# Performance work log

Measured on AMD Instinct MI355X. Metric: run time of the kernel, lower is better.

## Reference

```python
import jax, jax.numpy as jnp
import numpy as np

VOCAB = 50257
SOFT_CAP = 30.0
Z_LOSS_COEF = 1e-4
IGNORE_INDEX = -100


def setup_inputs() -> dict:
    key = jax.random.key(0)
    k1, k2, k3 = jax.random.split(key, 3)
    B, S, H = 2, 2048, 1024
    hidden = jax.random.normal(k1, (B, S, H), dtype=jnp.float32)
    lm_head_weight = jax.random.normal(k2, (VOCAB, H), dtype=jnp.float32) * 0.02
    labels = jax.random.randint(k3, (B, S), 0, VOCAB, dtype=jnp.int64)
    return {"hidden": hidden, "lm_head_weight": lm_head_weight, "labels": labels}


def reference(hidden, lm_head_weight, labels):
    # lm_head matmul: [B,S,H] x [V,H] -> [B,S,V]
    logits = jnp.einsum("bsh,vh->bsv", hidden, lm_head_weight)
    # Gemma-style tanh soft-cap
    logits = jnp.tanh(logits / SOFT_CAP) * SOFT_CAP
    # shift for next-token prediction
    shift_logits = logits[:, :-1].astype(jnp.float32)          # [B,S-1,V]
    shift_labels = labels[:, 1:]                               # [B,S-1]
    flat_logits = shift_logits.reshape(-1, VOCAB)              # [N,V]
    flat_labels = shift_labels.reshape(-1)                     # [N]
    valid = flat_labels != IGNORE_INDEX
    safe_labels = jnp.where(valid, flat_labels, 0)
    log_z = jax.nn.logsumexp(flat_logits, axis=-1)             # [N]
    picked = jnp.take_along_axis(flat_logits, safe_labels[:, None], axis=-1)[:, 0]
    nll = log_z - picked                                       # [N]
    n_valid = jnp.maximum(jnp.sum(valid), 1)
    ce = jnp.sum(jnp.where(valid, nll, 0.0)) / n_valid
    # z-loss: mean over valid tokens of logsumexp^2
    z_loss = ZLC = Z_LOSS_COEF * jnp.sum(jnp.where(valid, log_z ** 2, 0.0)) / n_valid
    return ce + z_loss
```

## Files before the change

kernel.cpp:

```cpp
#include <hip/hip_runtime.h>
#include <hip/hip_bf16.h>

#define VOCAB 50257
#define NPAD  50432
#define MROWS 4096
#define SEQ   2048
#define KDIM  1024
#define NT    16

typedef __attribute__((ext_vector_type(4))) float f32x4;
typedef __attribute__((ext_vector_type(8))) short bf16x8;

#define AS1 __attribute__((address_space(1)))
#define AS3 __attribute__((address_space(3)))

__device__ __forceinline__ void bar() {
  asm volatile("" ::: "memory");
  __builtin_amdgcn_s_barrier();
  asm volatile("" ::: "memory");
}

__device__ __forceinline__ unsigned int f2bf_pair(float lo, float hi) {
  unsigned int a = __float_as_uint(lo);
  a = (a + 0x7FFFu + ((a >> 16) & 1u)) >> 16;
  unsigned int b = __float_as_uint(hi);
  b = (b + 0x7FFFu + ((b >> 16) & 1u)) >> 16;
  return a | (b << 16);
}

__global__ void cast_hidden_k(const float* __restrict__ src, uint4* __restrict__ dst) {
  int i = blockIdx.x * 256 + threadIdx.x;
  const float4* s = ((const float4*)src) + (size_t)i * 2;
  float4 a = s[0], b = s[1];
  uint4 o;
  o.x = f2bf_pair(a.x, a.y);
  o.y = f2bf_pair(a.z, a.w);
  o.z = f2bf_pair(b.x, b.y);
  o.w = f2bf_pair(b.z, b.w);
  dst[i] = o;
}

__global__ void cast_weight_k(const float* __restrict__ src, uint4* __restrict__ dst) {
  int i = blockIdx.x * 256 + threadIdx.x;
  int row = i >> 7;
  uint4 o = make_uint4(0u, 0u, 0u, 0u);
  if (row < VOCAB) {
    const float4* s = ((const float4*)src) + (size_t)i * 2;
    float4 a = s[0], b = s[1];
    o.x = f2bf_pair(a.x, a.y);
    o.y = f2bf_pair(a.z, a.w);
    o.z = f2bf_pair(b.x, b.y);
    o.w = f2bf_pair(b.z, b.w);
  }
  dst[i] = o;
}

#define STAGE_X(base, h, bufb, isB, kt) do { \
  const unsigned short* _g = (base) + (size_t)((h)*128 + w*8) * KDIM + (kt)*64; \
  unsigned short* _l = LDS_ + (bufb) + (isB)*16384 + (h)*8192 + w*512; \
  __builtin_amdgcn_global_load_lds((const AS1 void*)_g, (AS3 void*)_l, 16, 0, 0); \
  __builtin_amdgcn_global_load_lds((const AS1 void*)(_g + (size_t)64*KDIM), (AS3 void*)(_l + 4096), 16, 0, 0); \
} while (0)

__global__ __launch_bounds__(512, 2) void gemm_ce_k(
    const unsigned short* __restrict__ A,
    const unsigned short* __restrict__ W,
    const int* __restrict__ labels,
    float* __restrict__ row_sum,
    float* __restrict__ picked)
{
  __shared__ __align__(16) unsigned short LDS_[65536];

  const int bid  = blockIdx.x;
  const int wg   = (bid & 7) * 394 + (bid >> 3);
  const int mblk = wg & 15;
  const int nblk = wg >> 4;
  const int tid  = threadIdx.x;
  const int lane = tid & 63;
  const int w    = tid >> 6;
  const int wm   = w >> 2;
  const int wn   = w & 3;

  const int arow0 = mblk * 256;
  const int wrow0 = nblk * 256;

  const int lrow = lane >> 3;
  const int lcol = ((lane & 7) * 8) ^ ((lane >> 3) << 3);
  const unsigned short* Abase = A + (size_t)(arow0 + lrow) * KDIM + lcol;
  const unsigned short* Wbase = W + (size_t)(wrow0 + lrow) * KDIM + lcol;

  const int rbase = (lane & 15) * 64 + (lane >> 4) * 8;
  const int xorm  = (lane & 7) << 3;

  f32x4 acc[8][4];
#pragma unroll
  for (int m = 0; m < 8; ++m)
#pragma unroll
    for (int n = 0; n < 4; ++n) acc[m][n] = (f32x4){0.f, 0.f, 0.f, 0.f};

  STAGE_X(Abase, 0, 0, 0, 0);
  STAGE_X(Abase, 1, 0, 0, 0);
  STAGE_X(Wbase, 0, 0, 1, 0);
  STAGE_X(Wbase, 1, 0, 1, 0);
  STAGE_X(Abase, 0, 32768, 0, 1);
  STAGE_X(Abase, 1, 32768, 0, 1);
  asm volatile("s_waitcnt vmcnt(4)" ::: "memory");
  bar();

  bf16x8 Af[2][4][2], Bf[2][2][2];

  for (int t = 0; t < NT; ++t) {
    const int cb = (t & 1) << 15;
    const int nb = cb ^ 32768;

#pragma unroll
    for (int a = 0; a < 4; ++a)
#pragma unroll
      for (int ks = 0; ks < 2; ++ks)
        Af[0][a][ks] = *(const bf16x8*)&LDS_[cb + (((wm*128 + a*16)*64 + rbase + ks*32) ^ xorm)];
#pragma unroll
    for (int b2 = 0; b2 < 2; ++b2)
#pragma unroll
      for (int ks = 0; ks < 2; ++ks)
        Bf[0][b2][ks] = *(const bf16x8*)&LDS_[cb + 16384 + (((wn*64 + b2*16)*64 + rbase + ks*32) ^ xorm)];
    if (t + 1 < NT) STAGE_X(Wbase, 0, nb, 1, t + 1);
    bar();
    __builtin_amdgcn_s_setprio(1);
#pragma unroll
    for (int a = 0; a < 4; ++a)
#pragma unroll
      for (int b2 = 0; b2 < 2; ++b2) {
        acc[a][b2] = __builtin_amdgcn_mfma_f32_16x16x32_bf16(Af[0][a][0], Bf[0][b2][0], acc[a][b2], 0, 0, 0);
        acc[a][b2] = __builtin_amdgcn_mfma_f32_16x16x32_bf16(Af[0][a][1], Bf[0][b2][1], acc[a][b2], 0, 0, 0);
      }
    __builtin_amdgcn_s_setprio(0);
    bar();

#pragma unroll
    for (int a = 0; a < 4; ++a)
#pragma unroll
      for (int ks = 0; ks < 2; ++ks)
        Af[1][a][ks] = *(const bf16x8*)&LDS_[cb + (((wm*128 + 64 + a*16)*64 + rbase + ks*32) ^ xorm)];
#pragma unroll
    for (int b2 = 0; b2 < 2; ++b2)
#pragma unroll
      for (int ks = 0; ks < 2; ++ks)
        Bf[1][b2][ks] = *(const bf16x8*)&LDS_[cb + 16384 + (((wn*64 + 32 + b2*16)*64 + rbase + ks*32) ^ xorm)];
    if (t + 1 < NT) STAGE_X(Wbase, 1, nb, 1, t + 1);
    bar();
    __builtin_amdgcn_s_setprio(1);
#pragma unroll
    for (int a = 0; a < 4; ++a)
#pragma unroll
      for (int b2 = 0; b2 < 2; ++b2) {
        acc[a][2+b2] = __builtin_amdgcn_mfma_f32_16x16x32_bf16(Af[0][a][0], Bf[1][b2][0], acc[a][2+b2], 0, 0, 0);
        acc[a][2+b2] = __builtin_amdgcn_mfma_f32_16x16x32_bf16(Af[0][a][1], Bf[1][b2][1], acc[a][2+b2], 0, 0, 0);
      }
    __builtin_amdgcn_s_setprio(0);
    bar();

    if (t + 2 < NT) STAGE_X(Abase, 0, cb, 0, t + 2);
    bar();
    __builtin_amdgcn_s_setprio(1);
#pragma unroll
    for (int a = 0; a < 4; ++a)
#pragma unroll
      for (int b2 = 0; b2 < 2; ++b2) {
        acc[4+a][b2] = __builtin_amdgcn_mfma_f32_16x16x32_bf16(Af[1][a][0], Bf[0][b2][0], acc[4+a][b2], 0, 0, 0);
        acc[4+a][b2] = __builtin_amdgcn_mfma_f32_16x16x32_bf16(Af[1][a][1], Bf[0][b2][1], acc[4+a][b2], 0, 0, 0);
      }
    __builtin_amdgcn_s_setprio(0);
    bar();

    if (t + 2 < NT) STAGE_X(Abase, 1, cb, 0, t + 2);
    bar();
    __builtin_amdgcn_s_setprio(1);
#pragma unroll
    for (int a = 0; a < 4; ++a)
#pragma unroll
      for (int b2 = 0; b2 < 2; ++b2) {
        acc[4+a][2+b2] = __builtin_amdgcn_mfma_f32_16x16x32_bf16(Af[1][a][0], Bf[1][b2][0], acc[4+a][2+b2], 0, 0, 0);
        acc[4+a][2+b2] = __builtin_amdgcn_mfma_f32_16x16x32_bf16(Af[1][a][1], Bf[1][b2][1], acc[4+a][2+b2], 0, 0, 0);
      }
    __builtin_amdgcn_s_setprio(0);
    if (t < NT - 2) { asm volatile("s_waitcnt vmcnt(4)" ::: "memory"); }
    else           { asm volatile("s_waitcnt vmcnt(0)" ::: "memory"); }
    bar();
  }

  const int arow_w = arow0 + wm * 128;
  const int vcol_w = wrow0 + wn * 64;
#pragma unroll
  for (int m8 = 0; m8 < 8; ++m8) {
#pragma unroll
    for (int r = 0; r < 4; ++r) {
      const int grow = arow_w + m8 * 16 + (lane >> 4) * 4 + r;
      int lab = -1;
      if ((grow & (SEQ - 1)) != (SEQ - 1)) lab = labels[grow + 1];
      float s = 0.f;
#pragma unroll
      for (int n4 = 0; n4 < 4; ++n4) {
        const int v = vcol_w + n4 * 16 + (lane & 15);
        const float z = acc[m8][n4][r];
        const float e2 = __expf(z * (2.f / 30.f));
        const float capped = 30.f * (1.f - 2.f * __builtin_amdgcn_rcpf(e2 + 1.f));
        if (v == lab) picked[grow] = capped;
        s += (v < VOCAB) ? __expf(capped) : 0.f;
      }
      s += __shfl_xor(s, 1);
      s += __shfl_xor(s, 2);
      s += __shfl_xor(s, 4);
      s += __shfl_xor(s, 8);
      if ((lane & 15) == 0) atomicAdd(&row_sum[grow], s);
    }
  }
}

__global__ void reduce_k(const int* __restrict__ labels, const float* __restrict__ row_sum,
                         const float* __restrict__ picked, float* __restrict__ out)
{
  const int tid = threadIdx.x;
  float ce = 0.f, zl = 0.f;
  int cnt = 0;
  for (int r = tid; r < MROWS; r += 256) {
    if ((r & (SEQ - 1)) == (SEQ - 1)) continue;
    const int lab = labels[r + 1];
    if (lab == -100) continue;
    const float lz = __logf(row_sum[r]);
    ce += lz - picked[r];
    zl += lz * lz;
    ++cnt;
  }
  __shared__ float sce[4], szl[4];
  __shared__ int scnt[4];
#pragma unroll
  for (int off = 32; off > 0; off >>= 1) {
    ce  += __shfl_down(ce, off);
    zl  += __shfl_down(zl, off);
    cnt += __shfl_down(cnt, off);
  }
  const int wv = tid >> 6;
  if ((tid & 63) == 0) { sce[wv] = ce; szl[wv] = zl; scnt[wv] = cnt; }
  __syncthreads();
  if (tid == 0) {
    float C = 0.f, Z = 0.f;
    int N = 0;
    for (int i = 0; i < 4; ++i) { C += sce[i]; Z += szl[i]; N += scnt[i]; }
    if (N < 1) N = 1;
    out[0] = C / N + 1e-4f * (Z / N);
  }
}

extern "C" void kernel_launch(void* const* d_in, const int* in_sizes, int n_in,
                              void* d_out, int out_size, void* d_ws, size_t ws_size,
                              hipStream_t stream) {
  const float* hidden = (const float*)d_in[0];
  const float* weight = (const float*)d_in[1];
  const int*   labels = (const int*)d_in[2];
  float* out = (float*)d_out;

  const size_t A_BYTES = (size_t)MROWS * KDIM * 2;
  const size_t W_BYTES = (size_t)NPAD * KDIM * 2;
  const size_t NEEDED  = A_BYTES + W_BYTES + 2 * MROWS * sizeof(float);
  if (ws_size < NEEDED) return;

  char* ws = (char*)d_ws;
  unsigned short* Abf = (unsigned short*)ws;
  unsigned short* Wbf = (unsigned short*)(ws + A_BYTES);
  float* row_sum = (float*)(ws + A_BYTES + W_BYTES);
  float* picked  = row_sum + MROWS;

  hipMemsetAsync(row_sum, 0, MROWS * sizeof(float), stream);
  cast_hidden_k<<<MROWS * KDIM / 8 / 256, 256, 0, stream>>>(hidden, (uint4*)Abf);
  cast_weight_k<<<NPAD * KDIM / 8 / 256, 256, 0, stream>>>(weight, (uint4*)Wbf);
  gemm_ce_k<<<16 * 197 , 512, 0, stream>>>(Abf, Wbf, labels, row_sum, picked);
  reduce_k<<<1, 256, 0, stream>>>(labels, row_sum, picked, out);
}
```

Before: 947.2 us.

## Replace per-row atomics with per-block partial sums and trim A-fragment registers

Result: faster. 812.6 us (-14.2%).

```diff
diff --git a/kernel.cpp b/kernel.cpp
--- a/kernel.cpp
+++ b/kernel.cpp
@@ -3,6 +3,7 @@
 
 #define VOCAB 50257
 #define NPAD  50432
+#define NBLKS 197
 #define MROWS 4096
 #define SEQ   2048
 #define KDIM  1024
@@ -62,11 +63,11 @@
   __builtin_amdgcn_global_load_lds((const AS1 void*)(_g + (size_t)64*KDIM), (AS3 void*)(_l + 4096), 16, 0, 0); \
 } while (0)
 
-__global__ __launch_bounds__(512, 2) void gemm_ce_k(
+__global__ __launch_bounds__(512) void gemm_ce_k(
     const unsigned short* __restrict__ A,
     const unsigned short* __restrict__ W,
     const int* __restrict__ labels,
-    float* __restrict__ row_sum,
+    float* __restrict__ partial,
     float* __restrict__ picked)
 {
   __shared__ __align__(16) unsigned short LDS_[65536];
@@ -107,8 +108,9 @@
   asm volatile("s_waitcnt vmcnt(4)" ::: "memory");
   bar();
 
-  bf16x8 Af[2][4][2], Bf[2][2][2];
-
+  bf16x8 Af[4][2], Bf[2][2][2];
+
+#pragma unroll 1
   for (int t = 0; t < NT; ++t) {
     const int cb = (t & 1) << 15;
     const int nb = cb ^ 32768;
@@ -117,7 +119,7 @@
     for (int a = 0; a < 4; ++a)
 #pragma unroll
       for (int ks = 0; ks < 2; ++ks)
-        Af[0][a][ks] = *(const bf16x8*)&LDS_[cb + (((wm*128 + a*16)*64 + rbase + ks*32) ^ xorm)];
+        Af[a][ks] = *(const bf16x8*)&LDS_[cb + (((wm*128 + a*16)*64 + rbase + ks*32) ^ xorm)];
 #pragma unroll
     for (int b2 = 0; b2 < 2; ++b2)
 #pragma unroll
@@ -130,17 +132,12 @@
     for (int a = 0; a < 4; ++a)
 #pragma unroll
       for (int b2 = 0; b2 < 2; ++b2) {
-        acc[a][b2] = __builtin_amdgcn_mfma_f32_16x16x32_bf16(Af[0][a][0], Bf[0][b2][0], acc[a][b2], 0, 0, 0);
-        acc[a][b2] = __builtin_amdgcn_mfma_f32_16x16x32_bf16(Af[0][a][1], Bf[0][b2][1], acc[a][b2], 0, 0, 0);
-      }
-    __builtin_amdgcn_s_setprio(0);
-    bar();
-
-#pragma unroll
-    for (int a = 0; a < 4; ++a)
-#pragma unroll
-      for (int ks = 0; ks < 2; ++ks)
-        Af[1][a][ks] = *(const bf16x8*)&LDS_[cb + (((wm*128 + 64 + a*16)*64 + rbase + ks*32) ^ xorm)];
+        acc[a][b2] = __builtin_amdgcn_mfma_f32_16x16x32_bf16(Af[a][0], Bf[0][b2][0], acc[a][b2], 0, 0, 0);
+        acc[a][b2] = __builtin_amdgcn_mfma_f32_16x16x32_bf16(Af[a][1], Bf[0][b2][1], acc[a][b2], 0, 0, 0);
+      }
+    __builtin_amdgcn_s_setprio(0);
+    bar();
+
 #pragma unroll
     for (int b2 = 0; b2 < 2; ++b2)
 #pragma unroll
@@ -153,12 +150,19 @@
     for (int a = 0; a < 4; ++a)
 #pragma unroll
       for (int b2 = 0; b2 < 2; ++b2) {
-        acc[a][2+b2] = __builtin_amdgcn_mfma_f32_16x16x32_bf16(Af[0][a][0], Bf[1][b2][0], acc[a][2+b2], 0, 0, 0);
-        acc[a][2+b2] = __builtin_amdgcn_mfma_f32_16x16x32_bf16(Af[0][a][1], Bf[1][b2][1], acc[a][2+b2], 0, 0, 0);
-      }
-    __builtin_amdgcn_s_setprio(0);
-    bar();
-
+        acc[a][2+b2] = __builtin_amdgcn_mfma_f32_16x16x32_bf16(Af[a][0], Bf[1][b2][0], acc[a][2+b2], 0, 0, 0);
+        acc[a][2+b2] = __builtin_amdgcn_mfma_f32_16x16x32_bf16(Af[a][1], Bf[1][b2][1], acc[a][2+b2], 0, 0, 0);
+      }
+    __builtin_amdgcn_s_setprio(0);
+    bar();
+
+#pragma unroll
+    for (int a = 0; a < 4; ++a)
+#pragma unroll
+      for (int ks = 0; ks < 2; ++ks)
+        Af[a][ks] = *(const bf16x8*)&LDS_[cb + (((wm*128 + 64 + a*16)*64 + rbase + ks*32) ^ xorm)];
+    asm volatile("s_waitcnt lgkmcnt(0)" ::: "memory");
+    __builtin_amdgcn_sched_barrier(0);
     if (t + 2 < NT) STAGE_X(Abase, 0, cb, 0, t + 2);
     bar();
     __builtin_amdgcn_s_setprio(1);
@@ -166,8 +170,8 @@
     for (int a = 0; a < 4; ++a)
 #pragma unroll
       for (int b2 = 0; b2 < 2; ++b2) {
-        acc[4+a][b2] = __builtin_amdgcn_mfma_f32_16x16x32_bf16(Af[1][a][0], Bf[0][b2][0], acc[4+a][b2], 0, 0, 0);
-        acc[4+a][b2] = __builtin_amdgcn_mfma_f32_16x16x32_bf16(Af[1][a][1], Bf[0][b2][1], acc[4+a][b2], 0, 0, 0);
+        acc[4+a][b2] = __builtin_amdgcn_mfma_f32_16x16x32_bf16(Af[a][0], Bf[0][b2][0], acc[4+a][b2], 0, 0, 0);
+        acc[4+a][b2] = __builtin_amdgcn_mfma_f32_16x16x32_bf16(Af[a][1], Bf[0][b2][1], acc[4+a][b2], 0, 0, 0);
       }
     __builtin_amdgcn_s_setprio(0);
     bar();
@@ -179,8 +183,8 @@
     for (int a = 0; a < 4; ++a)
 #pragma unroll
       for (int b2 = 0; b2 < 2; ++b2) {
-        acc[4+a][2+b2] = __builtin_amdgcn_mfma_f32_16x16x32_bf16(Af[1][a][0], Bf[1][b2][0], acc[4+a][2+b2], 0, 0, 0);
-        acc[4+a][2+b2] = __builtin_amdgcn_mfma_f32_16x16x32_bf16(Af[1][a][1], Bf[1][b2][1], acc[4+a][2+b2], 0, 0, 0);
+        acc[4+a][2+b2] = __builtin_amdgcn_mfma_f32_16x16x32_bf16(Af[a][0], Bf[1][b2][0], acc[4+a][2+b2], 0, 0, 0);
+        acc[4+a][2+b2] = __builtin_amdgcn_mfma_f32_16x16x32_bf16(Af[a][1], Bf[1][b2][1], acc[4+a][2+b2], 0, 0, 0);
       }
     __builtin_amdgcn_s_setprio(0);
     if (t < NT - 2) { asm volatile("s_waitcnt vmcnt(4)" ::: "memory"); }
@@ -188,6 +192,7 @@
     bar();
   }
 
+  float* red = (float*)LDS_;
   const int arow_w = arow0 + wm * 128;
   const int vcol_w = wrow0 + wn * 64;
 #pragma unroll
@@ -211,28 +216,33 @@
       s += __shfl_xor(s, 2);
       s += __shfl_xor(s, 4);
       s += __shfl_xor(s, 8);
-      if ((lane & 15) == 0) atomicAdd(&row_sum[grow], s);
+      if ((lane & 15) == 0) red[wn * 256 + (wm * 128 + m8 * 16 + (lane >> 4) * 4 + r)] = s;
     }
   }
-}
-
-__global__ void reduce_k(const int* __restrict__ labels, const float* __restrict__ row_sum,
-                         const float* __restrict__ picked, float* __restrict__ out)
+  bar();
+  if (tid < 256) {
+    float s = red[tid] + red[256 + tid] + red[512 + tid] + red[768 + tid];
+    partial[(size_t)nblk * MROWS + arow0 + tid] = s;
+  }
+}
+
+__global__ void reduce2_k(const int* __restrict__ labels, const float* __restrict__ partial,
+                          const float* __restrict__ picked, float* __restrict__ scal)
 {
   const int tid = threadIdx.x;
-  float ce = 0.f, zl = 0.f;
-  int cnt = 0;
-  for (int r = tid; r < MROWS; r += 256) {
-    if ((r & (SEQ - 1)) == (SEQ - 1)) continue;
-    const int lab = labels[r + 1];
-    if (lab == -100) continue;
-    const float lz = __logf(row_sum[r]);
-    ce += lz - picked[r];
-    zl += lz * lz;
-    ++cnt;
-  }
-  __shared__ float sce[4], szl[4];
-  __shared__ int scnt[4];
+  const int row = blockIdx.x * 256 + tid;
+  float ce = 0.f, zl = 0.f, cnt = 0.f;
+  int lab = -100;
+  if ((row & (SEQ - 1)) != (SEQ - 1)) lab = labels[row + 1];
+  if (lab != -100) {
+    float s = 0.f;
+    for (int p = 0; p < NBLKS; ++p) s += partial[(size_t)p * MROWS + row];
+    const float lz = __logf(s);
+    ce = lz - picked[row];
+    zl = lz * lz;
+    cnt = 1.f;
+  }
+  __shared__ float sm[3][4];
 #pragma unroll
   for (int off = 32; off > 0; off >>= 1) {
     ce  += __shfl_down(ce, off);
@@ -240,15 +250,18 @@
     cnt += __shfl_down(cnt, off);
   }
   const int wv = tid >> 6;
-  if ((tid & 63) == 0) { sce[wv] = ce; szl[wv] = zl; scnt[wv] = cnt; }
+  if ((tid & 63) == 0) { sm[0][wv] = ce; sm[1][wv] = zl; sm[2][wv] = cnt; }
   __syncthreads();
   if (tid == 0) {
-    float C = 0.f, Z = 0.f;
-    int N = 0;
-    for (int i = 0; i < 4; ++i) { C += sce[i]; Z += szl[i]; N += scnt[i]; }
-    if (N < 1) N = 1;
-    out[0] = C / N + 1e-4f * (Z / N);
-  }
+    atomicAdd(&scal[0], sm[0][0] + sm[0][1] + sm[0][2] + sm[0][3]);
+    atomicAdd(&scal[1], sm[1][0] + sm[1][1] + sm[1][2] + sm[1][3]);
+    atomicAdd(&scal[2], sm[2][0] + sm[2][1] + sm[2][2] + sm[2][3]);
+  }
+}
+
+__global__ void final_k(const float* __restrict__ scal, float* __restrict__ out) {
+  const float n = fmaxf(scal[2], 1.f);
+  out[0] = scal[0] / n + 1e-4f * (scal[1] / n);
 }
 
 extern "C" void kernel_launch(void* const* d_in, const int* in_sizes, int n_in,
@@ -261,18 +274,21 @@
 
   const size_t A_BYTES = (size_t)MROWS * KDIM * 2;
   const size_t W_BYTES = (size_t)NPAD * KDIM * 2;
-  const size_t NEEDED  = A_BYTES + W_BYTES + 2 * MROWS * sizeof(float);
+  const size_t P_BYTES = (size_t)NBLKS * MROWS * sizeof(float);
+  const size_t NEEDED  = A_BYTES + W_BYTES + P_BYTES + (MROWS + 4) * sizeof(float);
   if (ws_size < NEEDED) return;
 
   char* ws = (char*)d_ws;
   unsigned short* Abf = (unsigned short*)ws;
   unsigned short* Wbf = (unsigned short*)(ws + A_BYTES);
-  float* row_sum = (float*)(ws + A_BYTES + W_BYTES);
-  float* picked  = row_sum + MROWS;
-
-  hipMemsetAsync(row_sum, 0, MROWS * sizeof(float), stream);
+  float* partial = (float*)(ws + A_BYTES + W_BYTES);
+  float* picked  = partial + (size_t)NBLKS * MROWS;
+  float* scal    = picked + MROWS;
+
+  hipMemsetAsync(scal, 0, 3 * sizeof(float), stream);
   cast_hidden_k<<<MROWS * KDIM / 8 / 256, 256, 0, stream>>>(hidden, (uint4*)Abf);
   cast_weight_k<<<NPAD * KDIM / 8 / 256, 256, 0, stream>>>(weight, (uint4*)Wbf);
-  gemm_ce_k<<<16 * 197 , 512, 0, stream>>>(Abf, Wbf, labels, row_sum, picked);
-  reduce_k<<<1, 256, 0, stream>>>(labels, row_sum, picked, out);
-}
+  gemm_ce_k<<<16 * NBLKS , 512, 0, stream>>>(Abf, Wbf, labels, partial, picked);
+  reduce2_k<<<MROWS / 256, 256, 0, stream>>>(labels, partial, picked, scal);
+  final_k<<<1, 1, 0, stream>>>(scal, out);
+}
```
